# Kernel optimization log

Hardware: AMD Instinct MI355X
Metric: run time of the kernel (lower is better)

The kernel has to match this reference:

```python
import jax, jax.numpy as jnp
import numpy as np

IN_FEATURES = 256
OUT_FEATURES = 64
ALPHA = 0.2  # leaky relu slope


def _xavier_uniform(key, shape, gain=1.414):
    fan_in, fan_out = shape[0], shape[1]
    limit = gain * np.sqrt(6.0 / (fan_in + fan_out))
    return jax.random.uniform(key, shape, jnp.float32, -limit, limit)


def setup_inputs() -> dict:
    key = jax.random.key(0)
    k_h, k_W, k_a = jax.random.split(key, 3)
    h = jax.random.normal(k_h, (8, 2048, IN_FEATURES), dtype=jnp.float32)
    W = _xavier_uniform(k_W, (IN_FEATURES, OUT_FEATURES))
    a = _xavier_uniform(k_a, (2 * OUT_FEATURES, 1))
    return {"h": h, "W": W, "a": a}


def reference(h, W, a):
    # h: [B, N, F_in], W: [F_in, D], a: [2D, 1]
    Wh = h @ W  # [B, N, D]
    D = Wh.shape[-1]
    a1 = a[:D, 0]   # attends to source node i (repeat_interleave side)
    a2 = a[D:, 0]   # attends to target node j (repeat side)
    f1 = Wh @ a1    # [B, N]
    f2 = Wh @ a2    # [B, N]
    # e[b, i, j] = leakyrelu(a1.Wh[b,i] + a2.Wh[b,j])  -- identical math to
    # the original's O(N^2 * 2D) repeat/concat, without materializing it.
    e = jax.nn.leaky_relu(f1[:, :, None] + f2[:, None, :], negative_slope=ALPHA)  # [B, N, N]
    # NOTE: original applies softmax over dim=1 (over i, per column j).
    attention = jax.nn.softmax(e, axis=1)  # [B, N, N]
    # dropout is identity in eval mode
    h_prime = jnp.einsum('bij,bjd->bid', attention, Wh)  # [B, N, D]
    return jax.nn.elu(h_prime)  # concat=True path
```

## Files before the change

kernel.cpp:

```cpp
#include <hip/hip_runtime.h>

#define B 8
#define N 2048
#define KF 256
#define DF 64
#define LOG2E 1.44269504088896340736f
#define NR 2049

typedef __attribute__((ext_vector_type(8))) short short8;
typedef __attribute__((ext_vector_type(4))) float float4v;

__device__ __forceinline__ float fexp2(float x) {
#if __has_builtin(__builtin_amdgcn_exp2f)
    return __builtin_amdgcn_exp2f(x);
#else
    return exp2f(x);
#endif
}
__device__ __forceinline__ float eluf(float x) {
    return x > 0.f ? x : fexp2(x * LOG2E) - 1.0f;
}
__device__ __forceinline__ short bf16r(float x) {
    unsigned u = __float_as_uint(x);
    return (short)((u + 0x8000u) >> 16);
}
__device__ __forceinline__ unsigned sortkey(float x) {
    unsigned u = __float_as_uint(x);
    return u ^ (((unsigned)((int)u >> 31)) | 0x80000000u);
}
#define DOT4(c, u, p) \
    p = fmaf(c.x, u.x, fmaf(c.y, u.y, fmaf(c.z, u.z, fmaf(c.w, u.w, p))));

__global__ __launch_bounds__(256) void k_wh(const float* __restrict__ h,
                                            const float* __restrict__ W,
                                            const float* __restrict__ a,
                                            float* __restrict__ Wh,
                                            float* __restrict__ f1,
                                            float* __restrict__ f2) {
    __shared__ __align__(16) unsigned char smem[34816];
    short* lwt  = (short*)smem;
    float* lv   = (float*)(smem + 32768);
    float* lred = (float*)smem;
    float* lp   = (float*)(smem + 16896);

    int t = threadIdx.x;
    int wv = t >> 6, lane = t & 63;
    int n15 = lane & 15, q = lane >> 4;
    int bx = blockIdx.x;

    const float* hr = h + ((long)bx * 32 + n15) * KF + wv * 64 + q * 8;
    float4 c0 = *(const float4*)(hr);
    float4 c1 = *(const float4*)(hr + 4);
    float4 c2 = *(const float4*)(hr + 32);
    float4 c3 = *(const float4*)(hr + 36);

    {
        const float4* wr4 = (const float4*)(W + t * DF);
        float s1 = 0.f, s2 = 0.f;
        #pragma unroll
        for (int c = 0; c < 16; c++) {
            float4 w4 = wr4[c];
            float4 a1v = *(const float4*)(a + 4 * c);
            float4 a2v = *(const float4*)(a + DF + 4 * c);
            lwt[(4 * c + 0) * 256 + t] = bf16r(w4.x);
            lwt[(4 * c + 1) * 256 + t] = bf16r(w4.y);
            lwt[(4 * c + 2) * 256 + t] = bf16r(w4.z);
            lwt[(4 * c + 3) * 256 + t] = bf16r(w4.w);
            s1 = fmaf(w4.x, a1v.x, fmaf(w4.y, a1v.y, fmaf(w4.z, a1v.z, fmaf(w4.w, a1v.w, s1))));
            s2 = fmaf(w4.x, a2v.x, fmaf(w4.y, a2v.y, fmaf(w4.z, a2v.z, fmaf(w4.w, a2v.w, s2))));
        }
        lv[t] = s1;
        lv[256 + t] = s2;
    }
    __syncthreads();

    const short* bq = lwt + n15 * 256 + wv * 64 + q * 8;
    short8 s0b0 = *(const short8*)(bq);
    short8 s0b1 = *(const short8*)(bq + 16 * 256);
    short8 s0b2 = *(const short8*)(bq + 32 * 256);
    short8 s0b3 = *(const short8*)(bq + 48 * 256);
    short8 s1b0 = *(const short8*)(bq + 32);
    short8 s1b1 = *(const short8*)(bq + 16 * 256 + 32);
    short8 s1b2 = *(const short8*)(bq + 32 * 256 + 32);
    short8 s1b3 = *(const short8*)(bq + 48 * 256 + 32);
    const float* vv = lv + wv * 64 + q * 8;
    float4 u00 = *(const float4*)(vv);
    float4 u01 = *(const float4*)(vv + 4);
    float4 u10 = *(const float4*)(vv + 32);
    float4 u11 = *(const float4*)(vv + 36);
    float4 x00 = *(const float4*)(vv + 256);
    float4 x01 = *(const float4*)(vv + 256 + 4);
    float4 x10 = *(const float4*)(vv + 256 + 32);
    float4 x11 = *(const float4*)(vv + 256 + 36);
    __syncthreads();

    #pragma unroll
    for (int rt = 0; rt < 2; rt++) {
        float4 m0, m1, m2, m3;
        if (rt < 1) {
            const float* hn = hr + 16 * KF;
            m0 = *(const float4*)(hn);
            m1 = *(const float4*)(hn + 4);
            m2 = *(const float4*)(hn + 32);
            m3 = *(const float4*)(hn + 36);
        }
        float p1 = 0.f, p2 = 0.f;
        DOT4(c0, u00, p1) DOT4(c1, u01, p1) DOT4(c2, u10, p1) DOT4(c3, u11, p1)
        DOT4(c0, x00, p2) DOT4(c1, x01, p2) DOT4(c2, x10, p2) DOT4(c3, x11, p2)

        short8 af0 = { bf16r(c0.x), bf16r(c0.y), bf16r(c0.z), bf16r(c0.w),
                       bf16r(c1.x), bf16r(c1.y), bf16r(c1.z), bf16r(c1.w) };
        short8 af1 = { bf16r(c2.x), bf16r(c2.y), bf16r(c2.z), bf16r(c2.w),
                       bf16r(c3.x), bf16r(c3.y), bf16r(c3.z), bf16r(c3.w) };
        float4v acc0 = {0.f, 0.f, 0.f, 0.f}, acc1 = acc0, acc2 = acc0, acc3 = acc0;
        acc0 = __builtin_amdgcn_mfma_f32_16x16x32_bf16(af0, s0b0, acc0, 0, 0, 0);
        acc0 = __builtin_amdgcn_mfma_f32_16x16x32_bf16(af1, s1b0, acc0, 0, 0, 0);
        acc1 = __builtin_amdgcn_mfma_f32_16x16x32_bf16(af0, s0b1, acc1, 0, 0, 0);
        acc1 = __builtin_amdgcn_mfma_f32_16x16x32_bf16(af1, s1b1, acc1, 0, 0, 0);
        acc2 = __builtin_amdgcn_mfma_f32_16x16x32_bf16(af0, s0b2, acc2, 0, 0, 0);
        acc2 = __builtin_amdgcn_mfma_f32_16x16x32_bf16(af1, s1b2, acc2, 0, 0, 0);
        acc3 = __builtin_amdgcn_mfma_f32_16x16x32_bf16(af0, s0b3, acc3, 0, 0, 0);
        acc3 = __builtin_amdgcn_mfma_f32_16x16x32_bf16(af1, s1b3, acc3, 0, 0, 0);

        #define STASH(nb, A)                                                  \
            {                                                                 \
                _Pragma("unroll")                                             \
                for (int r = 0; r < 4; r++)                                   \
                    lred[wv * 1056 + (q * 4 + r) * 66 + nb * 16 + n15] = A[r]; \
            }
        STASH(0, acc0) STASH(1, acc1) STASH(2, acc2) STASH(3, acc3)
        #undef STASH
        p1 += __shfl_xor(p1, 16, 64); p1 += __shfl_xor(p1, 32, 64);
        p2 += __shfl_xor(p2, 16, 64); p2 += __shfl_xor(p2, 32, 64);
        if (q == 0) { lp[wv * 16 + n15] = p1; lp[64 + wv * 16 + n15] = p2; }
        __syncthreads();

        long i0 = (long)bx * 32 + rt * 16;
        int d = t & 63, ig = t >> 6;
        int bb = (int)(i0 >> 11);
        int il = (int)(i0 & (N - 1));
        float s0 = 0.f, s1 = 0.f, s2 = 0.f, s3 = 0.f;
        #pragma unroll
        for (int w = 0; w < 4; w++) {
            const float* lr = lred + w * 1056 + (ig * 4) * 66 + d;
            s0 += lr[0]; s1 += lr[66]; s2 += lr[132]; s3 += lr[198];
        }
        float* wp = Wh + ((long)bb * N + il + ig * 4) * DF + d;
        wp[0]      = s0;
        wp[DF]     = s1;
        wp[2 * DF] = s2;
        wp[3 * DF] = s3;

        if (t < 16) {
            f1[i0 + t] = lp[t] + lp[16 + t] + lp[32 + t] + lp[48 + t];
        } else if (t < 32) {
            int tt = t + 48;
            f2[i0 + t - 16] = lp[tt] + lp[16 + tt] + lp[32 + tt] + lp[48 + tt];
        }
        __syncthreads();
        c0 = m0; c1 = m1; c2 = m2; c3 = m3;
    }
}

__global__ __launch_bounds__(512) void k_rank(const float* __restrict__ f1,
                                              const float* __restrict__ f2,
                                              int* __restrict__ si,
                                              float* __restrict__ gA,
                                              float* __restrict__ gsA,
                                              int* __restrict__ s1i,
                                              float2* __restrict__ e1pk,
                                              int* __restrict__ Rarr) {
    __shared__ __align__(16) float4 qv[2048];
    __shared__ unsigned u2[2048];
    __shared__ float rS1[8][64], rS1s[8][64];
    __shared__ int   rC1[8][64], rC2[8][64], rC4[8][64];

    int t = threadIdx.x;
    int b = blockIdx.y;
    int base = blockIdx.x * 64;
    const float* f1g = f1 + (long)b * N;
    const float* f2g = f2 + (long)b * N;

    #pragma unroll
    for (int r = 0; r < 4; r++) {
        int idx = t + r * 512;
        float v1 = f1g[idx], v2 = f2g[idx];
        qv[idx] = make_float4(v1, fexp2(v1 * LOG2E), fexp2(v1 * 0.2f * LOG2E), v2);
        u2[idx] = sortkey(v2);
    }
    __syncthreads();

    int jl = t & 63, qt = t >> 6;
    int j = base + jl;
    float4 qj = qv[j];
    unsigned uj = u2[j];
    unsigned u1j = sortkey(qj.x);
    float negf2 = -qj.w;
    int c1 = 0, c2 = 0, c4 = 0;
    float S1 = 0.f, S1s = 0.f;
    int p0 = qt * 256;
    #pragma unroll 4
    for (int p = p0; p < p0 + 256; p++) {
        float4 qa = qv[p];
        unsigned up = u2[p];
        unsigned u1p = sortkey(qa.x);
        c2 += (up < uj || (up == uj && p < j)) ? 1 : 0;
        c1 += (u1p > u1j || (u1p == u1j && p < j)) ? 1 : 0;
        bool cc = qa.x < negf2;
        c4 += cc ? 1 : 0;
        S1  += cc ? 0.f : qa.y;
        S1s += cc ? qa.z : 0.f;
    }
    rC1[qt][jl] = c1; rC2[qt][jl] = c2; rC4[qt][jl] = c4;
    rS1[qt][jl] = S1; rS1s[qt][jl] = S1s;
    __syncthreads();

    if (t < 64) {
        int j2 = base + t;
        float4 qj2 = qv[j2];
        int rank1 = 0, rank2 = 0, cnt4 = 0;
        float s1 = 0.f, s1s = 0.f;
        #pragma unroll
        for (int k = 0; k < 8; k++) {
            rank1 += rC1[k][t]; rank2 += rC2[k][t]; cnt4 += rC4[k][t];
            s1 += rS1[k][t];    s1s += rS1s[k][t];
        }
        float E2  = fexp2(qj2.w * LOG2E);
        float E2s = fexp2(qj2.w * 0.2f * LOG2E);
        float rr = 1.0f / (E2 * s1 + E2s * s1s);
        si [(long)b * N + rank2] = j2;
        gA [(long)b * N + rank2] = E2 * rr;
        gsA[(long)b * N + rank2] = E2s * rr;
        Rarr[(long)b * NR + rank2 + 1] = N - cnt4;
        s1i [(long)b * N + rank1] = j2;
        e1pk[(long)b * N + rank1] = make_float2(qj2.y, qj2.z);
        if (blockIdx.x == 0 && t == 0) Rarr[(long)b * NR] = 0;
    }
}

__global__ __launch_bounds__(256) void k_seg(const float* __restrict__ Wh,
                                             const int* __restrict__ si,
                                             const float* __restrict__ gA,
                                             const float* __restrict__ gsA,
                                             float* __restrict__ segG,
                                             float* __restrict__ segGs) {
    int t = threadIdx.x;
    int d = t & 63, sq = t >> 6;
    int seg = blockIdx.x * 4 + sq, b = blockIdx.y;
    const int*   sib = si  + (long)b * N;
    const float* ga  = gA  + (long)b * N;
    const float* gsa = gsA + (long)b * N;
    const float* whb = Wh + (((long)b) << 11) * DF;
    float sg = 0.f, sgs = 0.f;
    #pragma unroll 8
    for (int x = 0; x < 32; x++) {
        int p = seg * 32 + x;
        int r = sib[p];
        float wv = whb[r * DF + d];
        sg  = fmaf(ga[p],  wv, sg);
        sgs = fmaf(gsa[p], wv, sgs);
    }
    segG [(b * 64 + seg) * DF + d] = sg;
    segGs[(b * 64 + seg) * DF + d] = sgs;
}

__global__ __launch_bounds__(256) void k_tabout(const float* __restrict__ Wh,
                                                const int* __restrict__ si,
                                                const float* __restrict__ gA,
                                                const float* __restrict__ gsA,
                                                const float* __restrict__ segG,
                                                const float* __restrict__ segGs,
                                                const int* __restrict__ s1i,
                                                const float2* __restrict__ e1pk,
                                                const int* __restrict__ Rarr,
                                                float* __restrict__ out) {
    __shared__ float lPG[4][64], lPGs[4][64];
    __shared__ float lTG[4][64];
    __shared__ float wG[4][64],  wGs[4][64];
    int t = threadIdx.x;
    int d = t & 63, sub = t >> 6;
    int seg = blockIdx.x, b = blockIdx.y;

    const float* sgb  = segG  + (b * 64) * DF + d;
    const float* sgsb = segGs + (b * 64) * DF + d;
    float pg = 0.f, pgs = 0.f, tg = 0.f;
    #pragma unroll
    for (int k = 0; k < 16; k++) {
        int s = sub * 16 + k;
        float vg = sgb[s * DF], vgs = sgsb[s * DF];
        tg += vg;
        if (s < seg) { pg += vg; pgs += vgs; }
    }
    lPG[sub][d] = pg; lPGs[sub][d] = pgs;
    lTG[sub][d] = tg;

    int p0 = seg * 32 + sub * 8;
    const int*   sib = si  + (long)b * N;
    const float* ga  = gA  + (long)b * N;
    const float* gsa = gsA + (long)b * N;
    const float* whb = Wh + (((long)b) << 11) * DF;
    float rows[8], gv[8], gsv[8];
    float sg = 0.f, sgs = 0.f;
    #pragma unroll
    for (int x = 0; x < 8; x++) {
        int p = p0 + x;
        int r = sib[p];
        float wv = whb[r * DF + d];
        rows[x] = wv; gv[x] = ga[p]; gsv[x] = gsa[p];
        sg  = fmaf(gv[x],  wv, sg);
        sgs = fmaf(gsv[x], wv, sgs);
    }
    wG[sub][d] = sg; wGs[sub][d] = sgs;
    __syncthreads();

    float totG   = lTG[0][d] + lTG[1][d] + lTG[2][d] + lTG[3][d];
    float baseG  = lPG[0][d] + lPG[1][d] + lPG[2][d] + lPG[3][d];
    float baseGs = lPGs[0][d] + lPGs[1][d] + lPGs[2][d] + lPGs[3][d];
    #pragma unroll
    for (int k = 0; k < 3; k++) {
        if (k < sub) { baseG += wG[k][d]; baseGs += wGs[k][d]; }
    }

    const int*    Ra = Rarr + (long)b * NR;
    const int*    s1b = s1i + (long)b * N;
    const float2* e1b = e1pk + (long)b * N;
    float* ob = out + ((long)b * N) * DF + d;

    float rg = baseG, rgs = baseGs;
    #pragma unroll
    for (int x = 0; x < 8; x++) {
        int p = p0 + x;
        float ss = totG - rg;
        float ps = rgs;
        int r0 = __builtin_amdgcn_readfirstlane(Ra[p]);
        int r1 = __builtin_amdgcn_readfirstlane(Ra[p + 1]);
        for (int rr = r0; rr < r1; rr++) {
            int row = s1b[rr];
            float2 ee = e1b[rr];
            ob[(long)row * DF] = eluf(ee.x * ss + ee.y * ps);
        }
        rg  = fmaf(gv[x],  rows[x], rg);
        rgs = fmaf(gsv[x], rows[x], rgs);
    }
    if (seg == 63 && sub == 3) {
        float ps = rgs;
        int r0 = __builtin_amdgcn_readfirstlane(Ra[2048]);
        for (int rr = r0; rr < N; rr++) {
            int row = s1b[rr];
            float2 ee = e1b[rr];
            ob[(long)row * DF] = eluf(ee.y * ps);
        }
    }
}

extern "C" void kernel_launch(void* const* d_in, const int* in_sizes, int n_in,
                              void* d_out, int out_size, void* d_ws, size_t ws_size,
                              hipStream_t stream) {
    const float* h = (const float*)d_in[0];
    const float* W = (const float*)d_in[1];
    const float* a = (const float*)d_in[2];
    float* out = (float*)d_out;

    char* ws = (char*)d_ws;
    const size_t NB = (size_t)B * N;
    size_t off = 0;
    float*  Wh    = (float*) (ws + off); off += NB * DF * sizeof(float);
    float*  f1    = (float*) (ws + off); off += NB * sizeof(float);
    float*  f2    = (float*) (ws + off); off += NB * sizeof(float);
    float*  gA    = (float*) (ws + off); off += NB * sizeof(float);
    float*  gsA   = (float*) (ws + off); off += NB * sizeof(float);
    float2* e1pk  = (float2*)(ws + off); off += NB * sizeof(float2);
    int*    si    = (int*)   (ws + off); off += NB * sizeof(int);
    int*    s1i   = (int*)   (ws + off); off += NB * sizeof(int);
    int*    Rarr  = (int*)   (ws + off); off += (size_t)B * NR * sizeof(int);
    float*  segG  = (float*) (ws + off); off += (size_t)B * 64 * DF * sizeof(float);
    float*  segGs = (float*) (ws + off); off += (size_t)B * 64 * DF * sizeof(float);
    (void)off; (void)ws_size;

    k_wh    <<<NB / 32, 256, 0, stream>>>(h, W, a, Wh, f1, f2);
    k_rank  <<<dim3(N / 64, B), 512, 0, stream>>>(f1, f2, si, gA, gsA, s1i, e1pk, Rarr);
    k_seg   <<<dim3(16, B), 256, 0, stream>>>(Wh, si, gA, gsA, segG, segGs);
    k_tabout<<<dim3(64, B), 256, 0, stream>>>(Wh, si, gA, gsA, segG, segGs,
                                              s1i, e1pk, Rarr, out);
}
```

Baseline: 112.2 us.

## Replace O(N^2) rank counting with per-batch bitonic sort and prefix-sum binary search

The rank kernel, which counted ranks and partial exp sums by brute-force pairwise comparison across 256 blocks, is replaced by one 1024-thread block per batch. Each block bitonic-sorts the f1 and f2 keys in shared memory, builds prefix sums of exp(f1) and exp(0.2*f1), and finds each threshold by binary search. This cuts the work from quadratic to N log^2 N but launches only 8 blocks, uses many __syncthreads barriers, and sums floats in a different order.

```diff
diff --git a/kernel.cpp b/kernel.cpp
--- a/kernel.cpp
+++ b/kernel.cpp
@@ -27,6 +27,10 @@
 __device__ __forceinline__ unsigned sortkey(float x) {
     unsigned u = __float_as_uint(x);
     return u ^ (((unsigned)((int)u >> 31)) | 0x80000000u);
+}
+__device__ __forceinline__ float invkey(unsigned k) {
+    unsigned u = (k & 0x80000000u) ? (k ^ 0x80000000u) : ~k;
+    return __uint_as_float(u);
 }
 #define DOT4(c, u, p) \
     p = fmaf(c.x, u.x, fmaf(c.y, u.y, fmaf(c.z, u.z, fmaf(c.w, u.w, p))));
@@ -162,79 +166,115 @@
     }
 }
 
-__global__ __launch_bounds__(512) void k_rank(const float* __restrict__ f1,
-                                              const float* __restrict__ f2,
-                                              int* __restrict__ si,
-                                              float* __restrict__ gA,
-                                              float* __restrict__ gsA,
-                                              int* __restrict__ s1i,
-                                              float2* __restrict__ e1pk,
-                                              int* __restrict__ Rarr) {
-    __shared__ __align__(16) float4 qv[2048];
-    __shared__ unsigned u2[2048];
-    __shared__ float rS1[8][64], rS1s[8][64];
-    __shared__ int   rC1[8][64], rC2[8][64], rC4[8][64];
+__global__ __launch_bounds__(1024) void k_sort(const float* __restrict__ f1,
+                                               const float* __restrict__ f2,
+                                               int* __restrict__ si,
+                                               float* __restrict__ gA,
+                                               float* __restrict__ gsA,
+                                               int* __restrict__ s1i,
+                                               float2* __restrict__ e1pk,
+                                               int* __restrict__ Rarr) {
+    __shared__ unsigned long long A1[2048];
+    __shared__ unsigned long long A2[2048];
+    __shared__ float PS1[2049], PS1s[2049];
+    __shared__ float seg1[256], seg1s[256];
 
     int t = threadIdx.x;
-    int b = blockIdx.y;
-    int base = blockIdx.x * 64;
-    const float* f1g = f1 + (long)b * N;
-    const float* f2g = f2 + (long)b * N;
-
-    #pragma unroll
-    for (int r = 0; r < 4; r++) {
-        int idx = t + r * 512;
-        float v1 = f1g[idx], v2 = f2g[idx];
-        qv[idx] = make_float4(v1, fexp2(v1 * LOG2E), fexp2(v1 * 0.2f * LOG2E), v2);
-        u2[idx] = sortkey(v2);
-    }
-    __syncthreads();
-
-    int jl = t & 63, qt = t >> 6;
-    int j = base + jl;
-    float4 qj = qv[j];
-    unsigned uj = u2[j];
-    unsigned u1j = sortkey(qj.x);
-    float negf2 = -qj.w;
-    int c1 = 0, c2 = 0, c4 = 0;
-    float S1 = 0.f, S1s = 0.f;
-    int p0 = qt * 256;
-    #pragma unroll 4
-    for (int p = p0; p < p0 + 256; p++) {
-        float4 qa = qv[p];
-        unsigned up = u2[p];
-        unsigned u1p = sortkey(qa.x);
-        c2 += (up < uj || (up == uj && p < j)) ? 1 : 0;
-        c1 += (u1p > u1j || (u1p == u1j && p < j)) ? 1 : 0;
-        bool cc = qa.x < negf2;
-        c4 += cc ? 1 : 0;
-        S1  += cc ? 0.f : qa.y;
-        S1s += cc ? qa.z : 0.f;
-    }
-    rC1[qt][jl] = c1; rC2[qt][jl] = c2; rC4[qt][jl] = c4;
-    rS1[qt][jl] = S1; rS1s[qt][jl] = S1s;
-    __syncthreads();
-
-    if (t < 64) {
-        int j2 = base + t;
-        float4 qj2 = qv[j2];
-        int rank1 = 0, rank2 = 0, cnt4 = 0;
-        float s1 = 0.f, s1s = 0.f;
+    int b = blockIdx.x;
+    long bN = (long)b * N;
+
+    #pragma unroll
+    for (int r = 0; r < 2; r++) {
+        int e = t + r * 1024;
+        A1[e] = (((unsigned long long)sortkey(f1[bN + e])) << 32) | (unsigned)e;
+        A2[e] = (((unsigned long long)sortkey(f2[bN + e])) << 32) | (unsigned)e;
+    }
+    __syncthreads();
+
+    for (int k = 2; k <= 2048; k <<= 1) {
+        for (int j = k >> 1; j > 0; j >>= 1) {
+            int i1 = ((t & ~(j - 1)) << 1) | (t & (j - 1));
+            int i2 = i1 | j;
+            bool up = (i1 & k) == 0;
+            unsigned long long a = A1[i1], c = A1[i2];
+            if ((a > c) == up) { A1[i1] = c; A1[i2] = a; }
+            unsigned long long e = A2[i1], f = A2[i2];
+            if ((e > f) == up) { A2[i1] = f; A2[i2] = e; }
+            __syncthreads();
+        }
+    }
+
+    if (t < 256) {
+        float s = 0.f;
         #pragma unroll
-        for (int k = 0; k < 8; k++) {
-            rank1 += rC1[k][t]; rank2 += rC2[k][t]; cnt4 += rC4[k][t];
-            s1 += rS1[k][t];    s1s += rS1s[k][t];
-        }
-        float E2  = fexp2(qj2.w * LOG2E);
-        float E2s = fexp2(qj2.w * 0.2f * LOG2E);
-        float rr = 1.0f / (E2 * s1 + E2s * s1s);
-        si [(long)b * N + rank2] = j2;
-        gA [(long)b * N + rank2] = E2 * rr;
-        gsA[(long)b * N + rank2] = E2s * rr;
-        Rarr[(long)b * NR + rank2 + 1] = N - cnt4;
-        s1i [(long)b * N + rank1] = j2;
-        e1pk[(long)b * N + rank1] = make_float2(qj2.y, qj2.z);
-        if (blockIdx.x == 0 && t == 0) Rarr[(long)b * NR] = 0;
+        for (int x = 0; x < 8; x++) {
+            float v = invkey((unsigned)(A1[t * 8 + x] >> 32));
+            s += fexp2(v * LOG2E);
+        }
+        seg1[t] = s;
+    } else if (t < 512) {
+        int i = t - 256;
+        float s = 0.f;
+        #pragma unroll
+        for (int x = 0; x < 8; x++) {
+            float v = invkey((unsigned)(A1[i * 8 + x] >> 32));
+            s += fexp2(v * 0.2f * LOG2E);
+        }
+        seg1s[i] = s;
+    }
+    __syncthreads();
+    for (int s = 1; s < 256; s <<= 1) {
+        float v = 0.f;
+        if (t < 256) { if (t >= s) v = seg1[t - s]; }
+        else if (t < 512) { int i = t - 256; if (i >= s) v = seg1s[i - s]; }
+        __syncthreads();
+        if (t < 256) { if (t >= s) seg1[t] += v; }
+        else if (t < 512) { int i = t - 256; if (i >= s) seg1s[i] += v; }
+        __syncthreads();
+    }
+    #pragma unroll
+    for (int r = 0; r < 2; r++) {
+        int p = t + r * 1024;
+        int sg = p >> 3;
+        float b1 = (sg == 0) ? 0.f : seg1[sg - 1];
+        float b2 = (sg == 0) ? 0.f : seg1s[sg - 1];
+        for (int x = sg * 8; x < p; x++) {
+            float v = invkey((unsigned)(A1[x] >> 32));
+            b1 += fexp2(v * LOG2E);
+            b2 += fexp2(v * 0.2f * LOG2E);
+        }
+        PS1[p] = b1; PS1s[p] = b2;
+    }
+    if (t == 0) { PS1[2048] = seg1[255]; PS1s[2048] = seg1s[255]; Rarr[(long)b * NR] = 0; }
+    __syncthreads();
+
+    float tot1 = PS1[2048];
+    #pragma unroll
+    for (int r = 0; r < 2; r++) {
+        int p = t + r * 1024;
+        unsigned long long a2 = A2[p];
+        int jrow = (int)(a2 & 0xFFFFFFFFu);
+        float f2v = invkey((unsigned)(a2 >> 32));
+        float E2  = fexp2(f2v * LOG2E);
+        float E2s = fexp2(f2v * 0.2f * LOG2E);
+        unsigned tkey = sortkey(-f2v);
+        int lo = 0, hi = 2048;
+        while (lo < hi) {
+            int mid = (lo + hi) >> 1;
+            if ((unsigned)(A1[mid] >> 32) < tkey) lo = mid + 1; else hi = mid;
+        }
+        float S1  = tot1 - PS1[lo];
+        float S1s = PS1s[lo];
+        float rr = 1.0f / (E2 * S1 + E2s * S1s);
+        si [bN + p] = jrow;
+        gA [bN + p] = E2 * rr;
+        gsA[bN + p] = E2s * rr;
+        Rarr[(long)b * NR + p + 1] = N - lo;
+        int asc = 2047 - p;
+        unsigned long long a1 = A1[asc];
+        float f1v = invkey((unsigned)(a1 >> 32));
+        s1i [bN + p] = (int)(a1 & 0xFFFFFFFFu);
+        e1pk[bN + p] = make_float2(fexp2(f1v * LOG2E), fexp2(f1v * 0.2f * LOG2E));
     }
 }
 
@@ -378,7 +418,7 @@
     (void)off; (void)ws_size;
 
     k_wh    <<<NB / 32, 256, 0, stream>>>(h, W, a, Wh, f1, f2);
-    k_rank  <<<dim3(N / 64, B), 512, 0, stream>>>(f1, f2, si, gA, gsA, s1i, e1pk, Rarr);
+    k_sort  <<<dim3(B), 1024, 0, stream>>>(f1, f2, si, gA, gsA, s1i, e1pk, Rarr);
     k_seg   <<<dim3(16, B), 256, 0, stream>>>(Wh, si, gA, gsA, segG, segGs);
     k_tabout<<<dim3(64, B), 256, 0, stream>>>(Wh, si, gA, gsA, segG, segGs,
                                               s1i, e1pk, Rarr, out);
```

After: 123.2 us. 1.1x slower.

## Replace f1 sort with bucket placement by threshold index and fuse into segment kernel

Applied to the files above, without the earlier changes.

The O(N^2) rank computation no longer produces a full sort of f1. Each node instead gets a bucket index, the count of f2 values below -f1, and a new block in the segment-sum kernel builds a histogram, prefix sums and scatter of s1i/e1pk from those buckets. Each k_rank thread now handles two columns to reuse the shared-memory loads, which halves the rank grid. The cost is serialized LDS atomics and a single block per batch doing the bucket scatter, and the order within a bucket becomes nondeterministic.

```diff
diff --git a/kernel.cpp b/kernel.cpp
--- a/kernel.cpp
+++ b/kernel.cpp
@@ -164,104 +164,157 @@
 
 __global__ __launch_bounds__(512) void k_rank(const float* __restrict__ f1,
                                               const float* __restrict__ f2,
+                                              int* __restrict__ tIdx,
                                               int* __restrict__ si,
                                               float* __restrict__ gA,
-                                              float* __restrict__ gsA,
-                                              int* __restrict__ s1i,
-                                              float2* __restrict__ e1pk,
-                                              int* __restrict__ Rarr) {
+                                              float* __restrict__ gsA) {
     __shared__ __align__(16) float4 qv[2048];
     __shared__ unsigned u2[2048];
-    __shared__ float rS1[8][64], rS1s[8][64];
-    __shared__ int   rC1[8][64], rC2[8][64], rC4[8][64];
+    __shared__ float rS1[8][128], rS1s[8][128];
+    __shared__ int   rC2[8][128], rC3[8][128];
 
     int t = threadIdx.x;
     int b = blockIdx.y;
-    int base = blockIdx.x * 64;
-    const float* f1g = f1 + (long)b * N;
-    const float* f2g = f2 + (long)b * N;
+    int base = blockIdx.x * 128;
+    long bN = (long)b * N;
 
     #pragma unroll
     for (int r = 0; r < 4; r++) {
         int idx = t + r * 512;
-        float v1 = f1g[idx], v2 = f2g[idx];
+        float v1 = f1[bN + idx], v2 = f2[bN + idx];
         qv[idx] = make_float4(v1, fexp2(v1 * LOG2E), fexp2(v1 * 0.2f * LOG2E), v2);
         u2[idx] = sortkey(v2);
     }
     __syncthreads();
 
     int jl = t & 63, qt = t >> 6;
-    int j = base + jl;
-    float4 qj = qv[j];
-    unsigned uj = u2[j];
-    unsigned u1j = sortkey(qj.x);
-    float negf2 = -qj.w;
-    int c1 = 0, c2 = 0, c4 = 0;
-    float S1 = 0.f, S1s = 0.f;
+    int ja = base + jl, jb = base + 64 + jl;
+    float4 qja = qv[ja], qjb = qv[jb];
+    unsigned uja = u2[ja], ujb = u2[jb];
+    float negf2a = -qja.w, negf1a = -qja.x;
+    float negf2b = -qjb.w, negf1b = -qjb.x;
+    int c2a = 0, c3a = 0, c2b = 0, c3b = 0;
+    float S1a = 0.f, S1sa = 0.f, S1b = 0.f, S1sb = 0.f;
     int p0 = qt * 256;
     #pragma unroll 4
     for (int p = p0; p < p0 + 256; p++) {
         float4 qa = qv[p];
         unsigned up = u2[p];
-        unsigned u1p = sortkey(qa.x);
-        c2 += (up < uj || (up == uj && p < j)) ? 1 : 0;
-        c1 += (u1p > u1j || (u1p == u1j && p < j)) ? 1 : 0;
-        bool cc = qa.x < negf2;
-        c4 += cc ? 1 : 0;
-        S1  += cc ? 0.f : qa.y;
-        S1s += cc ? qa.z : 0.f;
-    }
-    rC1[qt][jl] = c1; rC2[qt][jl] = c2; rC4[qt][jl] = c4;
-    rS1[qt][jl] = S1; rS1s[qt][jl] = S1s;
-    __syncthreads();
-
-    if (t < 64) {
+        c2a += (up < uja || (up == uja && p < ja)) ? 1 : 0;
+        c2b += (up < ujb || (up == ujb && p < jb)) ? 1 : 0;
+        bool ca = qa.x < negf2a;
+        bool cb = qa.x < negf2b;
+        S1a  += ca ? 0.f : qa.y;   S1sa += ca ? qa.z : 0.f;
+        S1b  += cb ? 0.f : qa.y;   S1sb += cb ? qa.z : 0.f;
+        c3a += (qa.w < negf1a) ? 1 : 0;
+        c3b += (qa.w < negf1b) ? 1 : 0;
+    }
+    rC2[qt][jl] = c2a;  rC2[qt][64 + jl] = c2b;
+    rC3[qt][jl] = c3a;  rC3[qt][64 + jl] = c3b;
+    rS1[qt][jl] = S1a;  rS1[qt][64 + jl] = S1b;
+    rS1s[qt][jl] = S1sa; rS1s[qt][64 + jl] = S1sb;
+    __syncthreads();
+
+    if (t < 128) {
         int j2 = base + t;
         float4 qj2 = qv[j2];
-        int rank1 = 0, rank2 = 0, cnt4 = 0;
+        int rank = 0, ti = 0;
         float s1 = 0.f, s1s = 0.f;
         #pragma unroll
         for (int k = 0; k < 8; k++) {
-            rank1 += rC1[k][t]; rank2 += rC2[k][t]; cnt4 += rC4[k][t];
-            s1 += rS1[k][t];    s1s += rS1s[k][t];
+            rank += rC2[k][t]; ti += rC3[k][t];
+            s1 += rS1[k][t];   s1s += rS1s[k][t];
         }
         float E2  = fexp2(qj2.w * LOG2E);
         float E2s = fexp2(qj2.w * 0.2f * LOG2E);
         float rr = 1.0f / (E2 * s1 + E2s * s1s);
-        si [(long)b * N + rank2] = j2;
-        gA [(long)b * N + rank2] = E2 * rr;
-        gsA[(long)b * N + rank2] = E2s * rr;
-        Rarr[(long)b * NR + rank2 + 1] = N - cnt4;
-        s1i [(long)b * N + rank1] = j2;
-        e1pk[(long)b * N + rank1] = make_float2(qj2.y, qj2.z);
-        if (blockIdx.x == 0 && t == 0) Rarr[(long)b * NR] = 0;
-    }
-}
-
-__global__ __launch_bounds__(256) void k_seg(const float* __restrict__ Wh,
-                                             const int* __restrict__ si,
-                                             const float* __restrict__ gA,
-                                             const float* __restrict__ gsA,
-                                             float* __restrict__ segG,
-                                             float* __restrict__ segGs) {
+        tIdx[bN + j2] = ti;
+        si [bN + rank] = j2;
+        gA [bN + rank] = E2 * rr;
+        gsA[bN + rank] = E2s * rr;
+    }
+}
+
+__global__ __launch_bounds__(256) void k_segbkt(const float* __restrict__ Wh,
+                                                const int* __restrict__ si,
+                                                const float* __restrict__ gA,
+                                                const float* __restrict__ gsA,
+                                                const float* __restrict__ f1,
+                                                const int* __restrict__ tIdx,
+                                                float* __restrict__ segG,
+                                                float* __restrict__ segGs,
+                                                int* __restrict__ s1i,
+                                                float2* __restrict__ e1pk,
+                                                int* __restrict__ Rarr) {
+    __shared__ int hist[2049];
+    __shared__ int Rl[2049];
+    __shared__ int part[256];
     int t = threadIdx.x;
-    int d = t & 63, sq = t >> 6;
-    int seg = blockIdx.x * 4 + sq, b = blockIdx.y;
-    const int*   sib = si  + (long)b * N;
-    const float* ga  = gA  + (long)b * N;
-    const float* gsa = gsA + (long)b * N;
-    const float* whb = Wh + (((long)b) << 11) * DF;
-    float sg = 0.f, sgs = 0.f;
-    #pragma unroll 8
-    for (int x = 0; x < 32; x++) {
-        int p = seg * 32 + x;
-        int r = sib[p];
-        float wv = whb[r * DF + d];
-        sg  = fmaf(ga[p],  wv, sg);
-        sgs = fmaf(gsa[p], wv, sgs);
-    }
-    segG [(b * 64 + seg) * DF + d] = sg;
-    segGs[(b * 64 + seg) * DF + d] = sgs;
+    int b = blockIdx.y;
+    int x = blockIdx.x;
+    long bN = (long)b * N;
+
+    if (x < 16) {
+        int d = t & 63, sq = t >> 6;
+        int seg = x * 4 + sq;
+        const int*   sib = si  + bN;
+        const float* ga  = gA  + bN;
+        const float* gsa = gsA + bN;
+        const float* whb = Wh + (((long)b) << 11) * DF;
+        float sg = 0.f, sgs = 0.f;
+        #pragma unroll 8
+        for (int k = 0; k < 32; k++) {
+            int p = seg * 32 + k;
+            int r = sib[p];
+            float wv = whb[r * DF + d];
+            sg  = fmaf(ga[p],  wv, sg);
+            sgs = fmaf(gsa[p], wv, sgs);
+        }
+        segG [(b * 64 + seg) * DF + d] = sg;
+        segGs[(b * 64 + seg) * DF + d] = sgs;
+        return;
+    }
+
+    for (int i = t; i < 2049; i += 256) hist[i] = 0;
+    __syncthreads();
+    int tis[8];
+    #pragma unroll
+    for (int r = 0; r < 8; r++) {
+        int i = t + r * 256;
+        int ti = tIdx[bN + i];
+        tis[r] = ti;
+        atomicAdd(&hist[ti], 1);
+    }
+    __syncthreads();
+    int s = 0;
+    #pragma unroll
+    for (int k = 0; k < 8; k++) s += hist[t * 8 + k];
+    part[t] = s;
+    __syncthreads();
+    for (int st = 1; st < 256; st <<= 1) {
+        int v = (t >= st) ? part[t - st] : 0;
+        __syncthreads();
+        part[t] += v;
+        __syncthreads();
+    }
+    int run = (t == 0) ? 0 : part[t - 1];
+    #pragma unroll
+    for (int k = 0; k < 8; k++) {
+        int p = t * 8 + k;
+        Rl[p] = run;
+        Rarr[(long)b * NR + p] = run;
+        run += hist[p];
+    }
+    if (t == 255) { Rl[2048] = run; Rarr[(long)b * NR + 2048] = run; }
+    __syncthreads();
+    #pragma unroll
+    for (int r = 0; r < 8; r++) {
+        int i = t + r * 256;
+        int slot = atomicAdd(&Rl[tis[r]], 1);
+        s1i[bN + slot] = i;
+        float v = f1[bN + i];
+        e1pk[bN + slot] = make_float2(fexp2(v * LOG2E), fexp2(v * 0.2f * LOG2E));
+    }
 }
 
 __global__ __launch_bounds__(256) void k_tabout(const float* __restrict__ Wh,
@@ -370,6 +423,7 @@
     float*  gA    = (float*) (ws + off); off += NB * sizeof(float);
     float*  gsA   = (float*) (ws + off); off += NB * sizeof(float);
     float2* e1pk  = (float2*)(ws + off); off += NB * sizeof(float2);
+    int*    tIdx  = (int*)   (ws + off); off += NB * sizeof(int);
     int*    si    = (int*)   (ws + off); off += NB * sizeof(int);
     int*    s1i   = (int*)   (ws + off); off += NB * sizeof(int);
     int*    Rarr  = (int*)   (ws + off); off += (size_t)B * NR * sizeof(int);
@@ -378,8 +432,9 @@
     (void)off; (void)ws_size;
 
     k_wh    <<<NB / 32, 256, 0, stream>>>(h, W, a, Wh, f1, f2);
-    k_rank  <<<dim3(N / 64, B), 512, 0, stream>>>(f1, f2, si, gA, gsA, s1i, e1pk, Rarr);
-    k_seg   <<<dim3(16, B), 256, 0, stream>>>(Wh, si, gA, gsA, segG, segGs);
+    k_rank  <<<dim3(N / 128, B), 512, 0, stream>>>(f1, f2, tIdx, si, gA, gsA);
+    k_segbkt<<<dim3(17, B), 256, 0, stream>>>(Wh, si, gA, gsA, f1, tIdx,
+                                              segG, segGs, s1i, e1pk, Rarr);
     k_tabout<<<dim3(64, B), 256, 0, stream>>>(Wh, si, gA, gsA, segG, segGs,
                                               s1i, e1pk, Rarr, out);
 }
```

New measurement: 116.7 us. 4.0% more time.
